# Kernel tuning notes

Hardware: AMD Instinct MI355X
Metric: run time of the kernel (lower is better)

## Reference

```python
import jax, jax.numpy as jnp
import numpy as np

LEAK = 0.01  # nn.LeakyReLU default slope


def _guide(x, w1, w3, b3, bias):
    # x: [N, 3, H, W]
    c_in = x.shape[1]
    x1 = jax.nn.leaky_relu(jnp.einsum('oi,nihw->nohw', w1[:, :, 0, 0], x), LEAK)
    x3 = jax.lax.conv_general_dilated(x, w3, (1, 1), 'SAME') + b3[None, :, None, None]
    x3 = jax.nn.leaky_relu(x3, LEAK)
    g = jnp.sum(x1 + x3, axis=1, keepdims=True) / c_in + bias[0]
    return jnp.clip(g, 0.0, 1.0)  # [N, 1, H, W]


def _slice(grid, guide):
    # grid: [N, C=12, D=12, GH=16, GW=16]; guide: [N, 1, H, W] in [0, 1]
    # Trilinear, align_corners=True grid_sample semantics.
    N, C, D, GH, GW = grid.shape
    H, W = guide.shape[2], guide.shape[3]
    fy = (jnp.arange(H, dtype=grid.dtype) / (H - 1)) * (GH - 1)   # [H]
    fx = (jnp.arange(W, dtype=grid.dtype) / (W - 1)) * (GW - 1)   # [W]
    fz = guide[:, 0] * (D - 1)                                    # [N, H, W]
    y0 = jnp.floor(fy).astype(jnp.int32); ty = fy - y0
    x0 = jnp.floor(fx).astype(jnp.int32); tx = fx - x0
    z0 = jnp.floor(fz).astype(jnp.int32); tz = fz - z0

    def slice_one(g, z0b, tzb):
        # g: [C, D, GH, GW]; z0b, tzb: [H, W]
        out = jnp.zeros((C, H, W), g.dtype)
        for dz in (0, 1):
            wz = (1.0 - tzb) if dz == 0 else tzb              # [H, W]
            zi = jnp.clip(z0b + dz, 0, D - 1)                 # [H, W]
            for dy in (0, 1):
                wy = (1.0 - ty) if dy == 0 else ty            # [H]
                yi = jnp.clip(y0 + dy, 0, GH - 1)             # [H]
                for dx in (0, 1):
                    wx = (1.0 - tx) if dx == 0 else tx        # [W]
                    xi = jnp.clip(x0 + dx, 0, GW - 1)         # [W]
                    corner = g[:, zi, yi[:, None], xi[None, :]]   # [C, H, W]
                    out = out + corner * (wz * wy[:, None] * wx[None, :])[None]
        return out

    return jax.vmap(slice_one)(grid, z0, tz)  # [N, 12, H, W]


def _apply(coeff, full):
    # coeff: [N, 12, H, W] -> 3x4 per-pixel affine on RGB
    N, _, H, W = coeff.shape
    c = coeff.reshape(N, 3, 4, H, W)
    return jnp.einsum('ncihw,nihw->nchw', c[:, :, :3], full) + c[:, :, 3]


def setup_inputs() -> dict:
    key = jax.random.key(0)
    ks = jax.random.split(key, 5)
    N, H, W = 4, 1024, 1024
    grid = jax.random.normal(ks[0], (N, 12, 12, 16, 16), jnp.float32)
    fullres = jax.random.uniform(ks[1], (N, 3, H, W), jnp.float32)
    # Guide conv1x1 initialized as identity + tiny noise (as in original)
    w1 = (jnp.eye(3, dtype=jnp.float32)
          + jax.random.normal(ks[2], (1,), jnp.float32)[0] * 1e-4).reshape(3, 3, 1, 1)
    w3 = jax.random.normal(ks[3], (3, 3, 3, 3), jnp.float32) * 0.1
    b3 = jax.random.normal(ks[4], (3,), jnp.float32) * 0.1
    guide_bias = jnp.zeros((1,), jnp.float32)
    return {"grid": grid, "fullres": fullres, "w1": w1, "w3": w3,
            "b3": b3, "guide_bias": guide_bias}


def reference(grid, fullres, w1, w3, b3, guide_bias):
    guide = _guide(fullres, w1, w3, b3, guide_bias)
    sliced = _slice(grid, guide)
    return _apply(sliced, fullres)
```

## Files before the change

### kernel.cpp

```cpp
#include <hip/hip_runtime.h>

#define LEAK 0.01f

typedef float v2f __attribute__((ext_vector_type(2)));
typedef _Float16 h2 __attribute__((ext_vector_type(2)));

constexpr int H = 1024, W = 1024, NIMG = 4;
constexpr int GC = 12, GD = 12, GH = 16, GW = 16;
constexpr int NZ = GD - 1;
constexpr int CELLE = NZ * GC;
constexpr int CF4 = 33;

constexpr int PX = 4;
constexpr int BX = 64, BY = 4;
constexpr int TILE_W = BX * PX;
constexpr int XS = 6;
constexpr int SGN = BY * XS * CF4;

constexpr int IMROWS = BY + 2;
constexpr int NCHUNK = 66;
constexpr int IMJW   = 68;

static __device__ __forceinline__ h2 bch2(float f) {
    return __builtin_bit_cast(h2, f);
}
static __device__ __forceinline__ float bcf(h2 v) {
    return __builtin_bit_cast(float, v);
}
static __device__ __forceinline__ h2 pkrtz(float a, float b) {
    return __builtin_bit_cast(h2, __builtin_amdgcn_cvt_pkrtz(a, b));
}

static __device__ __forceinline__ float fdot2f(h2 a, h2 b, float c) {
#if __has_builtin(__builtin_amdgcn_fdot2)
    return __builtin_amdgcn_fdot2(a, b, c, false);
#else
    return (float)a.x * (float)b.x + (float)a.y * (float)b.y + c;
#endif
}

__global__ __launch_bounds__(256) void pairgen(const float* __restrict__ grid,
                                               h2* __restrict__ table) {
    const int n  = blockIdx.x / NZ;
    const int z0 = blockIdx.x % NZ;
    const int yx = threadIdx.x;
    const float* src = grid + (size_t)n * GC * GD * GH * GW + yx;
    h2* dst = table + ((size_t)n * 256 + yx) * CELLE + z0 * GC;
    #pragma unroll
    for (int c = 0; c < GC; ++c) {
        float a = src[(c * GD + z0) * 256];
        float b = src[(c * GD + z0 + 1) * 256];
        dst[c] = pkrtz(a, b);
    }
}

__global__ __launch_bounds__(256) void hdrnet_fused(
    const float* __restrict__ grid,
    const float* __restrict__ full,
    const float* __restrict__ w1,
    const float* __restrict__ w3,
    const float* __restrict__ b3,
    const float* __restrict__ bias,
    const h2* __restrict__ table,
    float* __restrict__ out)
{
    __shared__ __align__(16) float simg[3 * IMROWS * 4 * IMJW];
    __shared__ __align__(16) h2 sgrid[BY * XS * CELLE];

    const int n  = blockIdx.z;
    const int wb = blockIdx.x * TILE_W;
    const int hb = blockIdx.y * BY;

    const float scale = 15.0f / 1023.0f;
    const int xlo = (int)(wb * scale);

    const int tid = threadIdx.y * BX + threadIdx.x;
    const size_t plane = (size_t)H * W;
    const float* fn = full + (size_t)n * 3 * plane;

    float4 tA[4], tB[4];
    const bool ttail = (tid < SGN - 768);
    if (table) {
        const float4* tsrc = (const float4*)(table + (size_t)n * 256 * CELLE);
        #pragma unroll
        for (int it = 0; it < 3; ++it) {
            int e  = tid + 256 * it;
            int r  = e / (XS * CF4);
            int t2 = e - r * (XS * CF4);
            int lx = t2 / CF4, q = t2 - lx * CF4;
            int y0 = min((int)((float)(hb + r) * scale), GH - 2);
            int xi = min(xlo + lx, GW - 1);
            tA[it] = tsrc[(y0 * GW + xi) * CF4 + q];
            tB[it] = tsrc[((y0 + 1) * GW + xi) * CF4 + q];
        }
        if (ttail) {
            int e  = 768 + tid;
            int r  = e / (XS * CF4);
            int t2 = e - r * (XS * CF4);
            int lx = t2 / CF4, q = t2 - lx * CF4;
            int y0 = min((int)((float)(hb + r) * scale), GH - 2);
            int xi = min(xlo + lx, GW - 1);
            tA[3] = tsrc[(y0 * GW + xi) * CF4 + q];
            tB[3] = tsrc[((y0 + 1) * GW + xi) * CF4 + q];
        }
    }

    for (int e = tid; e < 3 * IMROWS * NCHUNK; e += BX * BY) {
        int ch = e / (IMROWS * NCHUNK);
        int t  = e - ch * (IMROWS * NCHUNK);
        int r  = t / NCHUNK, m = t - r * NCHUNK;
        int yy = hb + r - 1;
        int gx = wb - 4 + 4 * m;
        float4 v = (float4){0.0f, 0.0f, 0.0f, 0.0f};
        if ((unsigned)yy < (unsigned)H && (unsigned)gx < (unsigned)W)
            v = *(const float4*)(fn + (size_t)ch * plane + (size_t)yy * W + gx);
        float* wp = &simg[((ch * IMROWS + r) * 4) * IMJW + m];
        wp[0 * IMJW] = v.x;
        wp[1 * IMJW] = v.y;
        wp[2 * IMJW] = v.z;
        wp[3 * IMJW] = v.w;
    }
    __syncthreads();

    if (table) {
        float4* sdst = (float4*)sgrid;
        #pragma unroll
        for (int it = 0; it < 4; ++it) {
            if (it == 3 && !ttail) break;
            int e = (it == 3) ? (768 + tid) : (tid + 256 * it);
            int r = e / (XS * CF4);
            float fy = (float)(hb + r) * scale;
            float ty = fy - (float)min((int)fy, GH - 2);
            _Float16 t1 = (_Float16)ty, t0 = (_Float16)(1.0f - ty);
            h2 w0v = (h2){t0, t0}, w1v = (h2){t1, t1};
            float4 A = tA[it], B = tB[it], R;
            R.x = bcf(bch2(A.x) * w0v + bch2(B.x) * w1v);
            R.y = bcf(bch2(A.y) * w0v + bch2(B.y) * w1v);
            R.z = bcf(bch2(A.z) * w0v + bch2(B.z) * w1v);
            R.w = bcf(bch2(A.w) * w0v + bch2(B.w) * w1v);
            sdst[e] = R;
        }
    } else {
        const float* gnn = grid + (size_t)n * GC * GD * GH * GW;
        for (int e = tid; e < BY * XS * CELLE; e += BX * BY) {
            int r  = e / (XS * CELLE);
            int t  = e - r * (XS * CELLE);
            int lx = t / CELLE, u = t - lx * CELLE;
            int z0 = u / GC, c = u - z0 * GC;
            float fy = (float)(hb + r) * scale;
            int y0 = min((int)fy, GH - 2);
            float ty = fy - (float)y0;
            int xi = min(xlo + lx, GW - 1);
            const float* gp = gnn + ((c * GD + z0) * GH + y0) * GW + xi;
            float a0 = gp[0],  a1 = gp[256];
            float b0 = gp[16], b1 = gp[272];
            sgrid[e] = pkrtz(fmaf(b0 - a0, ty, a0), fmaf(b1 - a1, ty, a1));
        }
    }

    const int h  = hb + threadIdx.y;
    const int w0 = wb + threadIdx.x * PX;

    float w1c[3][3];
    #pragma unroll
    for (int o = 0; o < 3; ++o)
        #pragma unroll
        for (int i = 0; i < 3; ++i)
            w1c[o][i] = w1[o * 3 + i];
    const float biasv = bias[0];

    v2f a3p[3][2];
    #pragma unroll
    for (int o = 0; o < 3; ++o) {
        float b = b3[o];
        a3p[o][0] = (v2f){b, b};
        a3p[o][1] = (v2f){b, b};
    }
    float rgb[3][PX];
    const int L = threadIdx.x;

    #pragma unroll
    for (int i = 0; i < 3; ++i) {
        #pragma unroll
        for (int dy = 0; dy < 3; ++dy) {
            const float* jp = &simg[((i * IMROWS + threadIdx.y + dy) * 4) * IMJW];
            float row[8];
            row[0] = jp[3 * IMJW + L];
            row[1] = jp[L + 1];
            row[2] = jp[1 * IMJW + L + 1];
            row[3] = jp[2 * IMJW + L + 1];
            row[4] = jp[3 * IMJW + L + 1];
            row[5] = jp[L + 2];
            row[6] = jp[1 * IMJW + L + 2];
            row[7] = jp[2 * IMJW + L + 2];
            if (dy == 1) {
                #pragma unroll
                for (int j = 0; j < PX; ++j) rgb[i][j] = row[1 + j];
            }
            #pragma unroll
            for (int o = 0; o < 3; ++o) {
                const float* kp = w3 + ((o * 3 + i) * 3 + dy) * 3;
                #pragma unroll
                for (int t = 0; t < 3; ++t) {
                    const float kt = kp[t];
                    v2f kv = (v2f){kt, kt};
                    a3p[o][0] = __builtin_elementwise_fma(
                        kv, (v2f){row[t], row[t + 1]}, a3p[o][0]);
                    a3p[o][1] = __builtin_elementwise_fma(
                        kv, (v2f){row[t + 2], row[t + 3]}, a3p[o][1]);
                }
            }
        }
    }
    __syncthreads();

    const int srow = threadIdx.y * XS;
    const float4* sg4 = (const float4*)sgrid;

    float4 ov0, ov1, ov2;
    float* ov0p = &ov0.x; float* ov1p = &ov1.x; float* ov2p = &ov2.x;

    #pragma unroll
    for (int j = 0; j < PX; ++j) {
        float gacc = 0.0f;
        #pragma unroll
        for (int o = 0; o < 3; ++o) {
            float x1 = fmaf(w1c[o][0], rgb[0][j],
                       fmaf(w1c[o][1], rgb[1][j], w1c[o][2] * rgb[2][j]));
            x1 = (x1 > 0.0f) ? x1 : LEAK * x1;
            float x3 = a3p[o][j >> 1][j & 1];
            x3 = (x3 > 0.0f) ? x3 : LEAK * x3;
            gacc += x1 + x3;
        }
        float g = fmaf(gacc, (1.0f / 3.0f), biasv);
        g = fminf(fmaxf(g, 0.0f), 1.0f);

        float fx = (float)(w0 + j) * scale;
        int x0 = (int)fx;
        x0 = min(x0, GW - 2);
        float tx = fx - (float)x0;
        const int lxr = x0 - xlo;

        float fz = g * 11.0f;
        int z0 = (int)fz;
        z0 = min(z0, GD - 2);
        float tz = fz - (float)z0;
        h2 hz = pkrtz(1.0f - tz, tz);
        _Float16 hx0 = (_Float16)(1.0f - tx), hx1 = (_Float16)tx;
        h2 wA = hz * (h2){hx0, hx0};
        h2 wB = hz * (h2){hx1, hx1};

        const float4* pA = sg4 + (srow + lxr) * CF4 + z0 * 3;
        const float4* pB = pA + CF4;
        float4 A0 = pA[0], A1 = pA[1], A2 = pA[2];
        float4 B0 = pB[0], B1 = pB[1], B2 = pB[2];

        float co[12];
        co[0]  = fdot2f(wA, bch2(A0.x), fdot2f(wB, bch2(B0.x), 0.0f));
        co[1]  = fdot2f(wA, bch2(A0.y), fdot2f(wB, bch2(B0.y), 0.0f));
        co[2]  = fdot2f(wA, bch2(A0.z), fdot2f(wB, bch2(B0.z), 0.0f));
        co[3]  = fdot2f(wA, bch2(A0.w), fdot2f(wB, bch2(B0.w), 0.0f));
        co[4]  = fdot2f(wA, bch2(A1.x), fdot2f(wB, bch2(B1.x), 0.0f));
        co[5]  = fdot2f(wA, bch2(A1.y), fdot2f(wB, bch2(B1.y), 0.0f));
        co[6]  = fdot2f(wA, bch2(A1.z), fdot2f(wB, bch2(B1.z), 0.0f));
        co[7]  = fdot2f(wA, bch2(A1.w), fdot2f(wB, bch2(B1.w), 0.0f));
        co[8]  = fdot2f(wA, bch2(A2.x), fdot2f(wB, bch2(B2.x), 0.0f));
        co[9]  = fdot2f(wA, bch2(A2.y), fdot2f(wB, bch2(B2.y), 0.0f));
        co[10] = fdot2f(wA, bch2(A2.z), fdot2f(wB, bch2(B2.z), 0.0f));
        co[11] = fdot2f(wA, bch2(A2.w), fdot2f(wB, bch2(B2.w), 0.0f));

        const float r = rgb[0][j], gg = rgb[1][j], b = rgb[2][j];
        ov0p[j] = fmaf(co[0], r, fmaf(co[1],  gg, fmaf(co[2],  b, co[3])));
        ov1p[j] = fmaf(co[4], r, fmaf(co[5],  gg, fmaf(co[6],  b, co[7])));
        ov2p[j] = fmaf(co[8], r, fmaf(co[9],  gg, fmaf(co[10], b, co[11])));
    }

    float* ob = out + (size_t)n * 3 * plane + (size_t)h * W + w0;
    *(float4*)(ob)             = ov0;
    *(float4*)(ob + plane)     = ov1;
    *(float4*)(ob + 2 * plane) = ov2;
}

extern "C" void kernel_launch(void* const* d_in, const int* in_sizes, int n_in,
                              void* d_out, int out_size, void* d_ws, size_t ws_size,
                              hipStream_t stream) {
    const float* grid_p = (const float*)d_in[0];
    const float* full_p = (const float*)d_in[1];
    const float* w1_p   = (const float*)d_in[2];
    const float* w3_p   = (const float*)d_in[3];
    const float* b3_p   = (const float*)d_in[4];
    const float* bias_p = (const float*)d_in[5];
    float* out_p = (float*)d_out;

    const size_t tbytes = (size_t)NIMG * 256 * CELLE * sizeof(h2);
    h2* table = (d_ws && ws_size >= tbytes) ? (h2*)d_ws : nullptr;

    if (table) {
        hipLaunchKernelGGL(pairgen, dim3(NIMG * NZ), dim3(256), 0, stream,
                           grid_p, table);
    }

    dim3 block(BX, BY, 1);
    dim3 grid_dim(W / TILE_W, H / BY, NIMG);
    hipLaunchKernelGGL(hdrnet_fused, grid_dim, block, 0, stream,
                       grid_p, full_p, w1_p, w3_p, b3_p, bias_p, table, out_p);
}
```

Baseline: 43.75 us.

## Reshape tile to 128x2 threads with two pixels each and new smem layout

```diff
diff --git a/kernel.cpp b/kernel.cpp
--- a/kernel.cpp
+++ b/kernel.cpp
@@ -11,15 +11,15 @@
 constexpr int CELLE = NZ * GC;
 constexpr int CF4 = 33;
 
-constexpr int PX = 4;
-constexpr int BX = 64, BY = 4;
+constexpr int PX = 2;
+constexpr int BX = 128, BY = 2;
 constexpr int TILE_W = BX * PX;
 constexpr int XS = 6;
 constexpr int SGN = BY * XS * CF4;
 
 constexpr int IMROWS = BY + 2;
 constexpr int NCHUNK = 66;
-constexpr int IMJW   = 68;
+constexpr int JW     = 132;
 
 static __device__ __forceinline__ h2 bch2(float f) {
     return __builtin_bit_cast(h2, f);
@@ -54,7 +54,7 @@
     }
 }
 
-__global__ __launch_bounds__(256) void hdrnet_fused(
+__global__ __launch_bounds__(256, 8) void hdrnet_fused(
     const float* __restrict__ grid,
     const float* __restrict__ full,
     const float* __restrict__ w1,
@@ -64,7 +64,7 @@
     const h2* __restrict__ table,
     float* __restrict__ out)
 {
-    __shared__ __align__(16) float simg[3 * IMROWS * 4 * IMJW];
+    __shared__ __align__(16) float simg[3 * IMROWS * 2 * JW];
     __shared__ __align__(16) h2 sgrid[BY * XS * CELLE];
 
     const int n  = blockIdx.z;
@@ -78,30 +78,29 @@
     const size_t plane = (size_t)H * W;
     const float* fn = full + (size_t)n * 3 * plane;
 
-    float4 tA[4], tB[4];
-    const bool ttail = (tid < SGN - 768);
+    float4 tA[2], tB[2];
+    const bool ttail = (tid < SGN - 256);
     if (table) {
         const float4* tsrc = (const float4*)(table + (size_t)n * 256 * CELLE);
-        #pragma unroll
-        for (int it = 0; it < 3; ++it) {
-            int e  = tid + 256 * it;
+        {
+            int e  = tid;
             int r  = e / (XS * CF4);
             int t2 = e - r * (XS * CF4);
             int lx = t2 / CF4, q = t2 - lx * CF4;
             int y0 = min((int)((float)(hb + r) * scale), GH - 2);
             int xi = min(xlo + lx, GW - 1);
-            tA[it] = tsrc[(y0 * GW + xi) * CF4 + q];
-            tB[it] = tsrc[((y0 + 1) * GW + xi) * CF4 + q];
+            tA[0] = tsrc[(y0 * GW + xi) * CF4 + q];
+            tB[0] = tsrc[((y0 + 1) * GW + xi) * CF4 + q];
         }
         if (ttail) {
-            int e  = 768 + tid;
+            int e  = 256 + tid;
             int r  = e / (XS * CF4);
             int t2 = e - r * (XS * CF4);
             int lx = t2 / CF4, q = t2 - lx * CF4;
             int y0 = min((int)((float)(hb + r) * scale), GH - 2);
             int xi = min(xlo + lx, GW - 1);
-            tA[3] = tsrc[(y0 * GW + xi) * CF4 + q];
-            tB[3] = tsrc[((y0 + 1) * GW + xi) * CF4 + q];
+            tA[1] = tsrc[(y0 * GW + xi) * CF4 + q];
+            tB[1] = tsrc[((y0 + 1) * GW + xi) * CF4 + q];
         }
     }
 
@@ -114,20 +113,21 @@
         float4 v = (float4){0.0f, 0.0f, 0.0f, 0.0f};
         if ((unsigned)yy < (unsigned)H && (unsigned)gx < (unsigned)W)
             v = *(const float4*)(fn + (size_t)ch * plane + (size_t)yy * W + gx);
-        float* wp = &simg[((ch * IMROWS + r) * 4) * IMJW + m];
-        wp[0 * IMJW] = v.x;
-        wp[1 * IMJW] = v.y;
-        wp[2 * IMJW] = v.z;
-        wp[3 * IMJW] = v.w;
+        float* j0 = &simg[((ch * IMROWS + r) * 2 + 0) * JW];
+        float* j1 = j0 + JW;
+        j0[2 * m]     = v.x;
+        j0[2 * m + 1] = v.z;
+        j1[2 * m]     = v.y;
+        j1[2 * m + 1] = v.w;
     }
     __syncthreads();
 
     if (table) {
         float4* sdst = (float4*)sgrid;
         #pragma unroll
-        for (int it = 0; it < 4; ++it) {
-            if (it == 3 && !ttail) break;
-            int e = (it == 3) ? (768 + tid) : (tid + 256 * it);
+        for (int it = 0; it < 2; ++it) {
+            if (it == 1 && !ttail) break;
+            int e = (it == 1) ? (256 + tid) : tid;
             int r = e / (XS * CF4);
             float fy = (float)(hb + r) * scale;
             float ty = fy - (float)min((int)fy, GH - 2);
@@ -159,7 +159,8 @@
     }
 
     const int h  = hb + threadIdx.y;
-    const int w0 = wb + threadIdx.x * PX;
+    const int L  = threadIdx.x;
+    const int w0 = wb + 2 * L;
 
     float w1c[3][3];
     #pragma unroll
@@ -169,33 +170,29 @@
             w1c[o][i] = w1[o * 3 + i];
     const float biasv = bias[0];
 
-    v2f a3p[3][2];
+    v2f a3p[3];
     #pragma unroll
     for (int o = 0; o < 3; ++o) {
         float b = b3[o];
-        a3p[o][0] = (v2f){b, b};
-        a3p[o][1] = (v2f){b, b};
-    }
-    float rgb[3][PX];
-    const int L = threadIdx.x;
+        a3p[o] = (v2f){b, b};
+    }
+    v2f rgbp[3];
 
     #pragma unroll
     for (int i = 0; i < 3; ++i) {
         #pragma unroll
         for (int dy = 0; dy < 3; ++dy) {
-            const float* jp = &simg[((i * IMROWS + threadIdx.y + dy) * 4) * IMJW];
-            float row[8];
-            row[0] = jp[3 * IMJW + L];
-            row[1] = jp[L + 1];
-            row[2] = jp[1 * IMJW + L + 1];
-            row[3] = jp[2 * IMJW + L + 1];
-            row[4] = jp[3 * IMJW + L + 1];
-            row[5] = jp[L + 2];
-            row[6] = jp[1 * IMJW + L + 2];
-            row[7] = jp[2 * IMJW + L + 2];
+            const float* j0 = &simg[((i * IMROWS + threadIdx.y + dy) * 2) * JW];
+            const float* j1 = j0 + JW;
+            float row[4];
+            row[0] = j1[L + 1];
+            row[1] = j0[L + 2];
+            row[2] = j1[L + 2];
+            row[3] = j0[L + 3];
             if (dy == 1) {
                 #pragma unroll
-                for (int j = 0; j < PX; ++j) rgb[i][j] = row[1 + j];
+                for (int i2 = 0; i2 < 1; ++i2) {}
+                rgbp[i] = (v2f){row[1], row[2]};
             }
             #pragma unroll
             for (int o = 0; o < 3; ++o) {
@@ -204,10 +201,8 @@
                 for (int t = 0; t < 3; ++t) {
                     const float kt = kp[t];
                     v2f kv = (v2f){kt, kt};
-                    a3p[o][0] = __builtin_elementwise_fma(
-                        kv, (v2f){row[t], row[t + 1]}, a3p[o][0]);
-                    a3p[o][1] = __builtin_elementwise_fma(
-                        kv, (v2f){row[t + 2], row[t + 3]}, a3p[o][1]);
+                    a3p[o] = __builtin_elementwise_fma(
+                        kv, (v2f){row[t], row[t + 1]}, a3p[o]);
                 }
             }
         }
@@ -217,18 +212,17 @@
     const int srow = threadIdx.y * XS;
     const float4* sg4 = (const float4*)sgrid;
 
-    float4 ov0, ov1, ov2;
-    float* ov0p = &ov0.x; float* ov1p = &ov1.x; float* ov2p = &ov2.x;
+    float ovv[3][PX];
 
     #pragma unroll
     for (int j = 0; j < PX; ++j) {
         float gacc = 0.0f;
         #pragma unroll
         for (int o = 0; o < 3; ++o) {
-            float x1 = fmaf(w1c[o][0], rgb[0][j],
-                       fmaf(w1c[o][1], rgb[1][j], w1c[o][2] * rgb[2][j]));
+            float x1 = fmaf(w1c[o][0], rgbp[0][j],
+                       fmaf(w1c[o][1], rgbp[1][j], w1c[o][2] * rgbp[2][j]));
             x1 = (x1 > 0.0f) ? x1 : LEAK * x1;
-            float x3 = a3p[o][j >> 1][j & 1];
+            float x3 = a3p[o][j];
             x3 = (x3 > 0.0f) ? x3 : LEAK * x3;
             gacc += x1 + x3;
         }
@@ -269,16 +263,16 @@
         co[10] = fdot2f(wA, bch2(A2.z), fdot2f(wB, bch2(B2.z), 0.0f));
         co[11] = fdot2f(wA, bch2(A2.w), fdot2f(wB, bch2(B2.w), 0.0f));
 
-        const float r = rgb[0][j], gg = rgb[1][j], b = rgb[2][j];
-        ov0p[j] = fmaf(co[0], r, fmaf(co[1],  gg, fmaf(co[2],  b, co[3])));
-        ov1p[j] = fmaf(co[4], r, fmaf(co[5],  gg, fmaf(co[6],  b, co[7])));
-        ov2p[j] = fmaf(co[8], r, fmaf(co[9],  gg, fmaf(co[10], b, co[11])));
+        const float r = rgbp[0][j], gg = rgbp[1][j], b = rgbp[2][j];
+        ovv[0][j] = fmaf(co[0], r, fmaf(co[1],  gg, fmaf(co[2],  b, co[3])));
+        ovv[1][j] = fmaf(co[4], r, fmaf(co[5],  gg, fmaf(co[6],  b, co[7])));
+        ovv[2][j] = fmaf(co[8], r, fmaf(co[9],  gg, fmaf(co[10], b, co[11])));
     }
 
     float* ob = out + (size_t)n * 3 * plane + (size_t)h * W + w0;
-    *(float4*)(ob)             = ov0;
-    *(float4*)(ob + plane)     = ov1;
-    *(float4*)(ob + 2 * plane) = ov2;
+    *(float2*)(ob)             = (float2){ovv[0][0], ovv[0][1]};
+    *(float2*)(ob + plane)     = (float2){ovv[1][0], ovv[1][1]};
+    *(float2*)(ob + 2 * plane) = (float2){ovv[2][0], ovv[2][1]};
 }
 
 extern "C" void kernel_launch(void* const* d_in, const int* in_sizes, int n_in,
```

After: 48.53 us. 10.9% more time.
